# Optimization experiments

Measured on AMD Instinct MI355X. Metric: run time of the kernel, lower is better.

The kernel has to match this reference:

```python
import jax, jax.numpy as jnp
import numpy as np

DIM = 768
NUM_HEADS = 12
HEAD_DIM = DIM // NUM_HEADS
SCALE = HEAD_DIM ** -0.5


def setup_inputs() -> dict:
    key = jax.random.key(0)
    ks = jax.random.split(key, 9)
    B, N = 2, 4096
    s = DIM ** -0.5
    return {
        "query": jax.random.normal(ks[0], (B, N, DIM), jnp.float32),
        "key": jax.random.normal(ks[1], (B, N, DIM), jnp.float32),
        "value": jax.random.normal(ks[2], (B, N, DIM), jnp.float32),
        "Wq": jax.random.normal(ks[3], (DIM, DIM), jnp.float32) * s,
        "Wk": jax.random.normal(ks[4], (DIM, DIM), jnp.float32) * s,
        "bk": jax.random.normal(ks[5], (DIM,), jnp.float32) * 0.02,
        "Wv": jax.random.normal(ks[6], (DIM, DIM), jnp.float32) * s,
        "Wp": jax.random.normal(ks[7], (DIM, DIM), jnp.float32) * s,
        "bp": jax.random.normal(ks[8], (DIM,), jnp.float32) * 0.02,
    }


def reference(query, key, value, Wq, Wk, bk, Wv, Wp, bp):
    B, Nq, C = query.shape
    Nk = key.shape[1]
    H, D = NUM_HEADS, HEAD_DIM
    # QKV projections (qv_bias=False -> no bias on q, v; k has bias)
    q = (query @ Wq.T).reshape(B, Nq, H, D).transpose(0, 2, 1, 3)  # [B,H,Nq,D]
    k = (key @ Wk.T + bk).reshape(B, Nk, H, D).transpose(0, 2, 1, 3)
    v = (value @ Wv.T).reshape(B, Nk, H, D).transpose(0, 2, 1, 3)
    # non-standard: exact GELU applied to K before QK^T
    k = jax.nn.gelu(k, approximate=False)
    attn = jnp.einsum("bhqd,bhkd->bhqk", q, k) * SCALE
    attn = jax.nn.softmax(attn, axis=-1)
    x = jnp.einsum("bhqk,bhkd->bhqd", attn, v)
    x = x.transpose(0, 2, 1, 3).reshape(B, Nq, C)
    return x @ Wp.T + bp
```

## Files before the change

kernel.cpp:

```cpp
#include <hip/hip_runtime.h>
#include <hip/hip_bf16.h>


#define DIM 768
#define NH 12
#define HD 64
#define NTOK 4096
#define WELEM 589824u
#define TELEM 6291456u

typedef short bf16x8 __attribute__((ext_vector_type(8)));
typedef float floatx4 __attribute__((ext_vector_type(4)));
typedef unsigned short us4 __attribute__((ext_vector_type(4)));

__device__ __forceinline__ float bf2f(unsigned short u) {
    union { unsigned int i; float f; } v; v.i = ((unsigned int)u) << 16; return v.f;
}
__device__ __forceinline__ unsigned short f2bf(float f) {
    union { float f; unsigned int i; } v; v.f = f;
    unsigned int r = v.i + 0x7fffu + ((v.i >> 16) & 1u);
    return (unsigned short)(r >> 16);
}
__device__ __forceinline__ void gl2lds16(const unsigned short* g, unsigned short* l) {
    __builtin_amdgcn_global_load_lds(
        (const __attribute__((address_space(1))) unsigned int*)g,
        (__attribute__((address_space(3))) unsigned int*)l, 16, 0, 0);
}
__device__ __forceinline__ bf16x8 ld8_f32_to_bf16(const float* p) {
    floatx4 f0 = *(const floatx4*)p;
    floatx4 f1 = *(const floatx4*)(p + 4);
    bf16x8 o;
    o[0] = (short)f2bf(f0[0]); o[1] = (short)f2bf(f0[1]);
    o[2] = (short)f2bf(f0[2]); o[3] = (short)f2bf(f0[3]);
    o[4] = (short)f2bf(f1[0]); o[5] = (short)f2bf(f1[1]);
    o[6] = (short)f2bf(f1[2]); o[7] = (short)f2bf(f1[3]);
    return o;
}

__global__ __launch_bounds__(256) void cvt_w(
    const float* __restrict__ a, const float* __restrict__ b,
    const float* __restrict__ c, const float* __restrict__ d,
    unsigned short* __restrict__ dst)
{
    size_t i = ((size_t)blockIdx.x * 256 + threadIdx.x) * 8;
    const float* s; size_t off;
    if (i < WELEM)            { s = a; off = i; }
    else if (i < 2u * WELEM)  { s = b; off = i - WELEM; }
    else if (i < 3u * WELEM)  { s = c; off = i - 2u * WELEM; }
    else                      { s = d; off = i - 3u * WELEM; }
    *(bf16x8*)(dst + i) = ld8_f32_to_bf16(s + off);
}

__global__ __launch_bounds__(256) void cvt_in(
    const float* __restrict__ a, const float* __restrict__ b,
    const float* __restrict__ c, unsigned short* __restrict__ dst)
{
    size_t i = ((size_t)blockIdx.x * 256 + threadIdx.x) * 8;
    const float* s; size_t off;
    if (i < TELEM)            { s = a; off = i; }
    else if (i < 2u * TELEM)  { s = b; off = i - TELEM; }
    else                      { s = c; off = i - 2u * TELEM; }
    *(bf16x8*)(dst + i) = ld8_f32_to_bf16(s + off);
}

template <int A_IS_BF16>
__device__ __forceinline__ void gemm128(
    const void* __restrict__ Av, const unsigned short* __restrict__ W,
    const float* __restrict__ bias, void* __restrict__ Cv,
    int has_bias, int do_gelu, int trans, int out_f32)
{
    __shared__ unsigned short As[128 * 64];
    __shared__ unsigned short Bs[128 * 64];
    const int m0 = blockIdx.x * 128, n0 = blockIdx.y * 128;
    const int tid = threadIdx.x;
    const int w = tid >> 6, l = tid & 63;
    const int g = l >> 4, r16 = l & 15;
    const int wm = w >> 1, wn = w & 1;
    const int ro = l >> 3, c = l & 7;
    const int cswz = ((c ^ ro) & 7) * 8;

    floatx4 acc[4][4];
#pragma unroll
    for (int i = 0; i < 4; i++)
#pragma unroll
        for (int j = 0; j < 4; j++) acc[i][j] = (floatx4){0.f, 0.f, 0.f, 0.f};

    for (int k0 = 0; k0 < DIM; k0 += 64) {
#pragma unroll
        for (int q = 0; q < 4; q++) {
            int rbase = w * 32 + q * 8;
            if (A_IS_BF16) {
                gl2lds16((const unsigned short*)Av + (size_t)(m0 + rbase + ro) * DIM + k0 + cswz,
                         As + rbase * 64);
            } else {
                bf16x8 a = ld8_f32_to_bf16((const float*)Av + (size_t)(m0 + rbase + ro) * DIM + k0 + c * 8);
                *(bf16x8*)(As + (rbase + ro) * 64 + cswz) = a;
            }
            gl2lds16(W + (size_t)(n0 + rbase + ro) * DIM + k0 + cswz, Bs + rbase * 64);
        }
        __syncthreads();

#pragma unroll
        for (int kk = 0; kk < 2; kk++) {
            bf16x8 af[4], bfr[4];
            int x = r16 & 7;
#pragma unroll
            for (int i = 0; i < 4; i++)
                af[i] = *(const bf16x8*)(As + (wm * 64 + i * 16 + r16) * 64 + (((kk * 4 + g) ^ x) * 8));
#pragma unroll
            for (int j = 0; j < 4; j++)
                bfr[j] = *(const bf16x8*)(Bs + (wn * 64 + j * 16 + r16) * 64 + (((kk * 4 + g) ^ x) * 8));
#pragma unroll
            for (int i = 0; i < 4; i++)
#pragma unroll
                for (int j = 0; j < 4; j++)
                    acc[i][j] = __builtin_amdgcn_mfma_f32_16x16x32_bf16(af[i], bfr[j], acc[i][j], 0, 0, 0);
        }
        __syncthreads();
    }

    if (trans) {
        unsigned short* C = (unsigned short*)Cv;
#pragma unroll
        for (int i = 0; i < 4; i++) {
            int m = m0 + wm * 64 + i * 16 + g * 4;
            int b = m >> 12, tloc = m & 4095;
#pragma unroll
            for (int j = 0; j < 4; j++) {
                int n = n0 + wn * 64 + j * 16 + r16;
                int h = n >> 6, d = n & 63;
                us4 pk;
                pk[0] = f2bf(acc[i][j][0]); pk[1] = f2bf(acc[i][j][1]);
                pk[2] = f2bf(acc[i][j][2]); pk[3] = f2bf(acc[i][j][3]);
                *(us4*)(C + ((size_t)(b * NH + h) * 64 + d) * NTOK + tloc) = pk;
            }
        }
    } else {
#pragma unroll
        for (int i = 0; i < 4; i++)
#pragma unroll
            for (int j = 0; j < 4; j++) {
                int n = n0 + wn * 64 + j * 16 + r16;
                float bv = has_bias ? bias[n] : 0.f;
#pragma unroll
                for (int r = 0; r < 4; r++) {
                    int m = m0 + wm * 64 + i * 16 + g * 4 + r;
                    float v = acc[i][j][r] + bv;
                    if (do_gelu) v = 0.5f * v * (1.f + erff(v * 0.70710678118f));
                    if (out_f32) ((float*)Cv)[(size_t)m * DIM + n] = v;
                    else ((unsigned short*)Cv)[(size_t)m * DIM + n] = f2bf(v);
                }
            }
    }
}

template <int A_IS_BF16>
__global__ __launch_bounds__(256) void qkv_gemm(
    const void* __restrict__ q_in, const void* __restrict__ k_in,
    const void* __restrict__ v_in,
    const unsigned short* __restrict__ Wq, const unsigned short* __restrict__ Wk,
    const unsigned short* __restrict__ Wv, const float* __restrict__ bk,
    unsigned short* __restrict__ Qo, unsigned short* __restrict__ Ko,
    unsigned short* __restrict__ Vto)
{
    int z = blockIdx.z;
    const void* A = (z == 0) ? q_in : (z == 1) ? k_in : v_in;
    const unsigned short* W = (z == 0) ? Wq : (z == 1) ? Wk : Wv;
    unsigned short* C = (z == 0) ? Qo : (z == 1) ? Ko : Vto;
    gemm128<A_IS_BF16>(A, W, bk, C, z == 1, z == 1, z == 2, 0);
}

__global__ __launch_bounds__(256) void out_gemm(
    const unsigned short* __restrict__ X, const unsigned short* __restrict__ Wp,
    const float* __restrict__ bp, float* __restrict__ out)
{
    gemm128<1>(X, Wp, bp, out, 1, 0, 0, 1);
}

__global__ __launch_bounds__(256) void attn_kernel(
    const unsigned short* __restrict__ Q, const unsigned short* __restrict__ K,
    const unsigned short* __restrict__ Vt, unsigned short* __restrict__ X)
{
    __shared__ unsigned short Ks[64 * 64];
    __shared__ unsigned short Vs[64 * 64];
    __shared__ unsigned short Ps[4 * 16 * 72];
    const int qt = blockIdx.x, bh = blockIdx.y;
    const int b = bh / NH, h = bh % NH;
    const int tid = threadIdx.x;
    const int w = tid >> 6, l = tid & 63;
    const int g = l >> 4, r16 = l & 15;
    const int tokbase = b * NTOK;

    const int qrow = tokbase + qt * 64 + w * 16 + r16;
    bf16x8 qf[2];
#pragma unroll
    for (int kk = 0; kk < 2; kk++) {
        qf[kk] = *(const bf16x8*)(Q + (size_t)qrow * DIM + h * HD + kk * 32 + g * 8);
#pragma unroll
        for (int j = 0; j < 8; j++)
            qf[kk][j] = (short)f2bf(bf2f((unsigned short)qf[kk][j]) * 0.125f);
    }

    floatx4 o[4];
#pragma unroll
    for (int dt = 0; dt < 4; dt++) o[dt] = (floatx4){0.f, 0.f, 0.f, 0.f};
    float lsum[4] = {0.f, 0.f, 0.f, 0.f};

    unsigned short* Pw = Ps + w * 16 * 72;
    const int ro = l >> 3, c = l & 7;
    const int cswz = ((c ^ ro) & 7) * 8;
    const int x = r16 & 7;

    for (int kt = 0; kt < NTOK / 64; kt++) {
#pragma unroll
        for (int is = 0; is < 2; is++) {
            int rloc = w * 8 + is * 32 + ro;
            gl2lds16(K + (size_t)(tokbase + kt * 64 + rloc) * DIM + h * HD + cswz,
                     Ks + (w * 8 + is * 32) * 64);
            gl2lds16(Vt + ((size_t)(b * NH + h) * 64 + rloc) * NTOK + kt * 64 + cswz,
                     Vs + (w * 8 + is * 32) * 64);
        }
        __syncthreads();

        floatx4 s[4];
#pragma unroll
        for (int ct = 0; ct < 4; ct++) {
            bf16x8 k0 = *(const bf16x8*)(Ks + (ct * 16 + r16) * 64 + ((g ^ x) * 8));
            bf16x8 k1 = *(const bf16x8*)(Ks + (ct * 16 + r16) * 64 + (((g + 4) ^ x) * 8));
            floatx4 z = (floatx4){0.f, 0.f, 0.f, 0.f};
            z = __builtin_amdgcn_mfma_f32_16x16x32_bf16(qf[0], k0, z, 0, 0, 0);
            s[ct] = __builtin_amdgcn_mfma_f32_16x16x32_bf16(qf[1], k1, z, 0, 0, 0);
        }

#pragma unroll
        for (int ct = 0; ct < 4; ct++)
#pragma unroll
            for (int r = 0; r < 4; r++) {
                float p = __expf(s[ct][r]);
                s[ct][r] = p;
                lsum[r] += p;
            }

#pragma unroll
        for (int ct = 0; ct < 4; ct++)
#pragma unroll
            for (int r = 0; r < 4; r++)
                Pw[(g * 4 + r) * 72 + ct * 16 + r16] = f2bf(s[ct][r]);

        bf16x8 pa0 = *(const bf16x8*)(Pw + r16 * 72 + g * 8);
        bf16x8 pa1 = *(const bf16x8*)(Pw + r16 * 72 + 32 + g * 8);
#pragma unroll
        for (int dt = 0; dt < 4; dt++) {
            bf16x8 v0 = *(const bf16x8*)(Vs + (dt * 16 + r16) * 64 + ((g ^ x) * 8));
            bf16x8 v1 = *(const bf16x8*)(Vs + (dt * 16 + r16) * 64 + (((g + 4) ^ x) * 8));
            o[dt] = __builtin_amdgcn_mfma_f32_16x16x32_bf16(pa0, v0, o[dt], 0, 0, 0);
            o[dt] = __builtin_amdgcn_mfma_f32_16x16x32_bf16(pa1, v1, o[dt], 0, 0, 0);
        }
        __syncthreads();
    }

#pragma unroll
    for (int off = 1; off < 16; off <<= 1)
#pragma unroll
        for (int r = 0; r < 4; r++)
            lsum[r] += __shfl_xor(lsum[r], off, 64);

#pragma unroll
    for (int r = 0; r < 4; r++) {
        float inv = 1.f / lsum[r];
        int tok = tokbase + qt * 64 + w * 16 + g * 4 + r;
#pragma unroll
        for (int dt = 0; dt < 4; dt++)
            X[(size_t)tok * DIM + h * HD + dt * 16 + r16] = f2bf(o[dt][r] * inv);
    }
}

extern "C" void kernel_launch(void* const* d_in, const int* in_sizes, int n_in,
                              void* d_out, int out_size, void* d_ws, size_t ws_size,
                              hipStream_t stream) {
    const float* query = (const float*)d_in[0];
    const float* key   = (const float*)d_in[1];
    const float* value = (const float*)d_in[2];
    const float* Wq    = (const float*)d_in[3];
    const float* Wk    = (const float*)d_in[4];
    const float* bk    = (const float*)d_in[5];
    const float* Wv    = (const float*)d_in[6];
    const float* Wp    = (const float*)d_in[7];
    const float* bp    = (const float*)d_in[8];
    float* out = (float*)d_out;

    unsigned short* ws = (unsigned short*)d_ws;
    unsigned short* Wqb = ws;
    unsigned short* Wkb = Wqb + WELEM;
    unsigned short* Wvb = Wkb + WELEM;
    unsigned short* Wpb = Wvb + WELEM;
    unsigned short* Qp  = Wpb + WELEM;
    unsigned short* Kp  = Qp + TELEM;
    unsigned short* Vtp = Kp + TELEM;
    unsigned short* Xp  = Vtp + TELEM;
    unsigned short* Qbf = Xp + TELEM;
    unsigned short* Kbf = Qbf + TELEM;
    unsigned short* Vbf = Kbf + TELEM;

    const size_t need_full = ((size_t)4 * WELEM + 7 * TELEM) * 2;
    const bool full = ws_size >= need_full;

    cvt_w<<<dim3(4 * WELEM / 8 / 256), 256, 0, stream>>>(Wq, Wk, Wv, Wp, Wqb);
    if (full) {
        cvt_in<<<dim3(3 * TELEM / 8 / 256), 256, 0, stream>>>(query, key, value, Qbf);
        qkv_gemm<1><<<dim3(64, 6, 3), 256, 0, stream>>>(Qbf, Kbf, Vbf, Wqb, Wkb, Wvb, bk, Qp, Kp, Vtp);
    } else {
        qkv_gemm<0><<<dim3(64, 6, 3), 256, 0, stream>>>(query, key, value, Wqb, Wkb, Wvb, bk, Qp, Kp, Vtp);
    }
    attn_kernel<<<dim3(64, 24), 256, 0, stream>>>(Qp, Kp, Vtp, Xp);
    out_gemm<<<dim3(64, 6), 256, 0, stream>>>(Xp, Wpb, bp, out);
}
```

Before: 370.5 us.

## Restructure attention: 2 waves with 64 queries each, transposed S, register P

The attention kernel now uses 128-thread blocks, and each wave handles 64 query rows (four 16-row fragments) instead of 16. K/V tiles are loaded once into registers and reused across the four fragments. QK^T is computed transposed (K as the A operand), so the P values land directly in the B-operand layout for the PV MFMA. This removes the LDS round trip for P. It also switches to exp2 with log2e folded into the Q scale, uses a new swizzle, splits loads so one wave loads K and the other V, and vectorizes output stores. Register pressure rises sharply (64 accumulator floats plus K/V fragments), and the grid has half as many blocks.

```diff
diff --git a/kernel.cpp b/kernel.cpp
--- a/kernel.cpp
+++ b/kernel.cpp
@@ -20,6 +20,12 @@
     union { float f; unsigned int i; } v; v.f = f;
     unsigned int r = v.i + 0x7fffu + ((v.i >> 16) & 1u);
     return (unsigned short)(r >> 16);
+}
+__device__ __forceinline__ unsigned int packbf(float a, float b) {
+    union { float f; unsigned int i; } ua, ub; ua.f = a; ub.f = b;
+    unsigned int ra = ua.i + 0x7fffu + ((ua.i >> 16) & 1u);
+    unsigned int rb = ub.i + 0x7fffu + ((ub.i >> 16) & 1u);
+    return __builtin_amdgcn_perm(rb, ra, 0x07060302);
 }
 __device__ __forceinline__ void gl2lds16(const unsigned short* g, unsigned short* l) {
     __builtin_amdgcn_global_load_lds(
@@ -37,6 +43,14 @@
     return o;
 }
 
+#if __has_builtin(__builtin_amdgcn_exp2f)
+#define EXPFN(x) __builtin_amdgcn_exp2f(x)
+#define QSCALE 0.18033688011f
+#else
+#define EXPFN(x) __expf(x)
+#define QSCALE 0.125f
+#endif
+
 __global__ __launch_bounds__(256) void cvt_w(
     const float* __restrict__ a, const float* __restrict__ b,
     const float* __restrict__ c, const float* __restrict__ d,
@@ -177,13 +191,14 @@
     gemm128<1>(X, Wp, bp, out, 1, 0, 0, 1);
 }
 
-__global__ __launch_bounds__(256) void attn_kernel(
+__device__ __forceinline__ int swzf(int R) { return (R & 7) ^ ((R >> 2) & 6); }
+
+__global__ __launch_bounds__(128, 2) void attn_kernel(
     const unsigned short* __restrict__ Q, const unsigned short* __restrict__ K,
     const unsigned short* __restrict__ Vt, unsigned short* __restrict__ X)
 {
     __shared__ unsigned short Ks[64 * 64];
     __shared__ unsigned short Vs[64 * 64];
-    __shared__ unsigned short Ps[4 * 16 * 72];
     const int qt = blockIdx.x, bh = blockIdx.y;
     const int b = bh / NH, h = bh % NH;
     const int tid = threadIdx.x;
@@ -191,87 +206,136 @@
     const int g = l >> 4, r16 = l & 15;
     const int tokbase = b * NTOK;
 
-    const int qrow = tokbase + qt * 64 + w * 16 + r16;
-    bf16x8 qf[2];
-#pragma unroll
-    for (int kk = 0; kk < 2; kk++) {
-        qf[kk] = *(const bf16x8*)(Q + (size_t)qrow * DIM + h * HD + kk * 32 + g * 8);
-#pragma unroll
-        for (int j = 0; j < 8; j++)
-            qf[kk][j] = (short)f2bf(bf2f((unsigned short)qf[kk][j]) * 0.125f);
-    }
-
-    floatx4 o[4];
-#pragma unroll
-    for (int dt = 0; dt < 4; dt++) o[dt] = (floatx4){0.f, 0.f, 0.f, 0.f};
+    bf16x8 qfr[4][2];
+#pragma unroll
+    for (int qfi = 0; qfi < 4; qfi++) {
+        int qrow = tokbase + qt * 128 + w * 64 + qfi * 16 + r16;
+#pragma unroll
+        for (int kk = 0; kk < 2; kk++) {
+            bf16x8 t = *(const bf16x8*)(Q + (size_t)qrow * DIM + h * HD + kk * 32 + g * 8);
+#pragma unroll
+            for (int j = 0; j < 8; j++)
+                t[j] = (short)f2bf(bf2f((unsigned short)t[j]) * QSCALE);
+            qfr[qfi][kk] = t;
+        }
+    }
+
+    int koff[4][2], voff[4][2];
+#pragma unroll
+    for (int ct = 0; ct < 4; ct++) {
+        int krow = (ct >> 1) * 32 + (r16 >> 2) * 8 + (ct & 1) * 4 + (r16 & 3);
+#pragma unroll
+        for (int kk = 0; kk < 2; kk++)
+            koff[ct][kk] = krow * 64 + (((kk * 4 + g) ^ swzf(krow)) * 8);
+    }
+#pragma unroll
+    for (int dt = 0; dt < 4; dt++) {
+        int vrow = dt * 16 + r16;
+#pragma unroll
+        for (int c = 0; c < 2; c++)
+            voff[dt][c] = vrow * 64 + (((c * 4 + g) ^ swzf(vrow)) * 8);
+    }
+
+    int soff[8];
+    const int srl = l >> 3, scc = l & 7;
+    const int sstride = (w == 0) ? DIM : NTOK;
+#pragma unroll
+    for (int i = 0; i < 8; i++) {
+        int row = i * 8 + srl;
+        soff[i] = row * sstride + ((scc ^ swzf(row)) * 8);
+    }
+    const unsigned short* Kbase = K + (size_t)tokbase * DIM + h * HD;
+    const unsigned short* Vbase = Vt + (size_t)bh * 64 * NTOK;
+
+    floatx4 o[4][4];
+#pragma unroll
+    for (int qfi = 0; qfi < 4; qfi++)
+#pragma unroll
+        for (int dt = 0; dt < 4; dt++) o[qfi][dt] = (floatx4){0.f, 0.f, 0.f, 0.f};
     float lsum[4] = {0.f, 0.f, 0.f, 0.f};
 
-    unsigned short* Pw = Ps + w * 16 * 72;
-    const int ro = l >> 3, c = l & 7;
-    const int cswz = ((c ^ ro) & 7) * 8;
-    const int x = r16 & 7;
-
     for (int kt = 0; kt < NTOK / 64; kt++) {
-#pragma unroll
-        for (int is = 0; is < 2; is++) {
-            int rloc = w * 8 + is * 32 + ro;
-            gl2lds16(K + (size_t)(tokbase + kt * 64 + rloc) * DIM + h * HD + cswz,
-                     Ks + (w * 8 + is * 32) * 64);
-            gl2lds16(Vt + ((size_t)(b * NH + h) * 64 + rloc) * NTOK + kt * 64 + cswz,
-                     Vs + (w * 8 + is * 32) * 64);
+        if (w == 0) {
+            const unsigned short* p = Kbase + (size_t)kt * 64 * DIM;
+#pragma unroll
+            for (int i = 0; i < 8; i++) gl2lds16(p + soff[i], Ks + i * 512);
+        } else {
+            const unsigned short* p = Vbase + kt * 64;
+#pragma unroll
+            for (int i = 0; i < 8; i++) gl2lds16(p + soff[i], Vs + i * 512);
         }
         __syncthreads();
 
-        floatx4 s[4];
-#pragma unroll
-        for (int ct = 0; ct < 4; ct++) {
-            bf16x8 k0 = *(const bf16x8*)(Ks + (ct * 16 + r16) * 64 + ((g ^ x) * 8));
-            bf16x8 k1 = *(const bf16x8*)(Ks + (ct * 16 + r16) * 64 + (((g + 4) ^ x) * 8));
-            floatx4 z = (floatx4){0.f, 0.f, 0.f, 0.f};
-            z = __builtin_amdgcn_mfma_f32_16x16x32_bf16(qf[0], k0, z, 0, 0, 0);
-            s[ct] = __builtin_amdgcn_mfma_f32_16x16x32_bf16(qf[1], k1, z, 0, 0, 0);
-        }
-
+        bf16x8 kr[4][2], vr[4][2];
 #pragma unroll
         for (int ct = 0; ct < 4; ct++)
 #pragma unroll
-            for (int r = 0; r < 4; r++) {
-                float p = __expf(s[ct][r]);
-                s[ct][r] = p;
-                lsum[r] += p;
-            }
-
-#pragma unroll
-        for (int ct = 0; ct < 4; ct++)
-#pragma unroll
-            for (int r = 0; r < 4; r++)
-                Pw[(g * 4 + r) * 72 + ct * 16 + r16] = f2bf(s[ct][r]);
-
-        bf16x8 pa0 = *(const bf16x8*)(Pw + r16 * 72 + g * 8);
-        bf16x8 pa1 = *(const bf16x8*)(Pw + r16 * 72 + 32 + g * 8);
+            for (int kk = 0; kk < 2; kk++)
+                kr[ct][kk] = *(const bf16x8*)(Ks + koff[ct][kk]);
+#pragma unroll
+        for (int dt = 0; dt < 4; dt++)
+#pragma unroll
+            for (int c = 0; c < 2; c++)
+                vr[dt][c] = *(const bf16x8*)(Vs + voff[dt][c]);
+
+#pragma unroll
+        for (int qfi = 0; qfi < 4; qfi++) {
+            floatx4 s[4];
+#pragma unroll
+            for (int ct = 0; ct < 4; ct++) {
+                floatx4 z = (floatx4){0.f, 0.f, 0.f, 0.f};
+                z = __builtin_amdgcn_mfma_f32_16x16x32_bf16(kr[ct][0], qfr[qfi][0], z, 0, 0, 0);
+                s[ct] = __builtin_amdgcn_mfma_f32_16x16x32_bf16(kr[ct][1], qfr[qfi][1], z, 0, 0, 0);
+            }
+            float ls = 0.f;
+#pragma unroll
+            for (int ct = 0; ct < 4; ct++)
+#pragma unroll
+                for (int r = 0; r < 4; r++) {
+                    float p = EXPFN(s[ct][r]);
+                    s[ct][r] = p;
+                    ls += p;
+                }
+            lsum[qfi] += ls;
+
+            unsigned int pk[4][2];
+#pragma unroll
+            for (int ct = 0; ct < 4; ct++) {
+                pk[ct][0] = packbf(s[ct][0], s[ct][1]);
+                pk[ct][1] = packbf(s[ct][2], s[ct][3]);
+            }
+#pragma unroll
+            for (int c = 0; c < 2; c++) {
+                union { unsigned int u[4]; bf16x8 v; } bf;
+                bf.u[0] = pk[2 * c][0]; bf.u[1] = pk[2 * c][1];
+                bf.u[2] = pk[2 * c + 1][0]; bf.u[3] = pk[2 * c + 1][1];
+#pragma unroll
+                for (int dt = 0; dt < 4; dt++)
+                    o[qfi][dt] = __builtin_amdgcn_mfma_f32_16x16x32_bf16(vr[dt][c], bf.v, o[qfi][dt], 0, 0, 0);
+            }
+        }
+        __syncthreads();
+    }
+
+#pragma unroll
+    for (int qfi = 0; qfi < 4; qfi++) {
+        lsum[qfi] += __shfl_xor(lsum[qfi], 16, 64);
+        lsum[qfi] += __shfl_xor(lsum[qfi], 32, 64);
+    }
+
+#pragma unroll
+    for (int qfi = 0; qfi < 4; qfi++) {
+        float inv = 1.f / lsum[qfi];
+        int tok = tokbase + qt * 128 + w * 64 + qfi * 16 + r16;
 #pragma unroll
         for (int dt = 0; dt < 4; dt++) {
-            bf16x8 v0 = *(const bf16x8*)(Vs + (dt * 16 + r16) * 64 + ((g ^ x) * 8));
-            bf16x8 v1 = *(const bf16x8*)(Vs + (dt * 16 + r16) * 64 + (((g + 4) ^ x) * 8));
-            o[dt] = __builtin_amdgcn_mfma_f32_16x16x32_bf16(pa0, v0, o[dt], 0, 0, 0);
-            o[dt] = __builtin_amdgcn_mfma_f32_16x16x32_bf16(pa1, v1, o[dt], 0, 0, 0);
-        }
-        __syncthreads();
-    }
-
-#pragma unroll
-    for (int off = 1; off < 16; off <<= 1)
-#pragma unroll
-        for (int r = 0; r < 4; r++)
-            lsum[r] += __shfl_xor(lsum[r], off, 64);
-
-#pragma unroll
-    for (int r = 0; r < 4; r++) {
-        float inv = 1.f / lsum[r];
-        int tok = tokbase + qt * 64 + w * 16 + g * 4 + r;
-#pragma unroll
-        for (int dt = 0; dt < 4; dt++)
-            X[(size_t)tok * DIM + h * HD + dt * 16 + r16] = f2bf(o[dt][r] * inv);
+            us4 pkv;
+            pkv[0] = f2bf(o[qfi][dt][0] * inv);
+            pkv[1] = f2bf(o[qfi][dt][1] * inv);
+            pkv[2] = f2bf(o[qfi][dt][2] * inv);
+            pkv[3] = f2bf(o[qfi][dt][3] * inv);
+            *(us4*)(X + (size_t)tok * DIM + h * HD + dt * 16 + g * 4) = pkv;
+        }
     }
 }
 
@@ -312,6 +376,6 @@
     } else {
         qkv_gemm<0><<<dim3(64, 6, 3), 256, 0, stream>>>(query, key, value, Wqb, Wkb, Wvb, bk, Qp, Kp, Vtp);
     }
-    attn_kernel<<<dim3(64, 24), 256, 0, stream>>>(Qp, Kp, Vtp, Xp);
+    attn_kernel<<<dim3(32, 24), 128, 0, stream>>>(Qp, Kp, Vtp, Xp);
     out_gemm<<<dim3(64, 6), 256, 0, stream>>>(Xp, Wpb, bp, out);
 }
```

Measured after the change: 353.6 us. 1.05x faster.
